# Performance work log

Measured on AMD Instinct MI355X. Metric: run time of the kernel, lower is better.

The kernel has to match this reference:

```python
import jax, jax.numpy as jnp
import numpy as np

N_BINS = 256
HOP = 80


def _gru(xs, Wih, Whh, bih, bhh, reverse=False):
    """Single-layer unidirectional GRU, PyTorch gate layout (r, z, n).
    xs: (T, B, I); Wih: (3H, I); Whh: (3H, H). Returns (T, B, H)."""
    H = Whh.shape[1]
    gi = jnp.einsum('tbi,gi->tbg', xs, Wih) + bih  # precompute input projections

    def step(h, gi_t):
        gh = h @ Whh.T + bhh
        ir, iz, inn = jnp.split(gi_t, 3, axis=-1)
        hr, hz, hn = jnp.split(gh, 3, axis=-1)
        r = jax.nn.sigmoid(ir + hr)
        z = jax.nn.sigmoid(iz + hz)
        n = jnp.tanh(inn + r * hn)
        h_new = (1.0 - z) * n + z * h
        return h_new, h_new

    h0 = jnp.zeros((xs.shape[1], H), xs.dtype)
    _, ys = jax.lax.scan(step, h0, gi, reverse=reverse)
    return ys


def _quantize(w):
    # continuous [-1, 1] -> bin index in [0, N_BINS-1]
    return jnp.clip(jnp.floor((w + 1.0) * (N_BINS / 2)), 0, N_BINS - 1).astype(jnp.int32)


def _forward(x, y, p):
    # --- encode: 2-layer bidirectional GRU over mel frames ---
    c = x
    for l in ('m0', 'm1'):
        f = _gru(c, p[l + 'f_Wih'], p[l + 'f_Whh'], p[l + 'f_bih'], p[l + 'f_bhh'])
        bwd = _gru(c, p[l + 'b_Wih'], p[l + 'b_Whh'], p[l + 'b_bih'], p[l + 'b_bhh'], reverse=True)
        c = jnp.concatenate([f, bwd], axis=-1)  # (t_m, b, 2*dim_enc)
    # nearest-neighbor upsample in time (matches F.interpolate default 'nearest')
    c = jnp.repeat(c, HOP, axis=0)  # (t_w, b, 2*dim_enc)

    # --- teacher forcing: shift waveform right, vectorize via embedding ---
    b = x.shape[1]
    w = jnp.concatenate([jnp.zeros((1, b), y.dtype), y[:-1]], axis=0)
    e = p['E'][_quantize(w)]  # (t_w, b, dim_vec)

    # --- wav GRU + projection + GELU ---
    o = _gru(jnp.concatenate([e, c], axis=-1), p['w_Wih'], p['w_Whh'], p['w_bih'], p['w_bhh'])
    o = jax.nn.gelu(o @ p['Wp'].T + p['bp'], approximate=False)  # (t_w, b, dim_proj)

    # --- categorical neg log prob over quantized targets ---
    logits = o @ p['Wd'].T + p['bd']  # (t_w, b, N_BINS)
    logp = jax.nn.log_softmax(logits, axis=-1)
    tgt = _quantize(y)
    nll = -jnp.mean(jnp.take_along_axis(logp, tgt[..., None], axis=-1))
    return nll


def setup_inputs() -> dict:
    key = jax.random.key(0)
    ks = iter(jax.random.split(key, 64))

    def rn(shape, s=0.08):
        return jax.random.normal(next(ks), shape, jnp.float32) * s

    t_m, b, dm = 32, 4, 80
    de, dv, dd, dp = 128, 256, 896, 512
    d = {}
    d['x'] = jax.random.normal(next(ks), (t_m, b, dm), jnp.float32)
    d['y'] = jax.random.uniform(next(ks), (t_m * HOP, b), jnp.float32, minval=-1.0, maxval=1.0)
    for name, i in [('m0f', dm), ('m0b', dm), ('m1f', 2 * de), ('m1b', 2 * de)]:
        d[name + '_Wih'] = rn((3 * de, i))
        d[name + '_Whh'] = rn((3 * de, de))
        d[name + '_bih'] = rn((3 * de,))
        d[name + '_bhh'] = rn((3 * de,))
    d['w_Wih'] = rn((3 * dd, 2 * de + dv))
    d['w_Whh'] = rn((3 * dd, dd))
    d['w_bih'] = rn((3 * dd,))
    d['w_bhh'] = rn((3 * dd,))
    d['Wp'] = rn((dp, dd))
    d['bp'] = rn((dp,))
    d['E'] = rn((N_BINS, dv))
    d['Wd'] = rn((N_BINS, dp))
    d['bd'] = rn((N_BINS,))
    return d


def reference(x, y, m0f_Wih, m0f_Whh, m0f_bih, m0f_bhh, m0b_Wih, m0b_Whh, m0b_bih, m0b_bhh,
              m1f_Wih, m1f_Whh, m1f_bih, m1f_bhh, m1b_Wih, m1b_Whh, m1b_bih, m1b_bhh,
              w_Wih, w_Whh, w_bih, w_bhh, Wp, bp, E, Wd, bd):
    p = dict(m0f_Wih=m0f_Wih, m0f_Whh=m0f_Whh, m0f_bih=m0f_bih, m0f_bhh=m0f_bhh,
             m0b_Wih=m0b_Wih, m0b_Whh=m0b_Whh, m0b_bih=m0b_bih, m0b_bhh=m0b_bhh,
             m1f_Wih=m1f_Wih, m1f_Whh=m1f_Whh, m1f_bih=m1f_bih, m1f_bhh=m1f_bhh,
             m1b_Wih=m1b_Wih, m1b_Whh=m1b_Whh, m1b_bih=m1b_bih, m1b_bhh=m1b_bhh,
             w_Wih=w_Wih, w_Whh=w_Whh, w_bih=w_bih, w_bhh=w_bhh,
             Wp=Wp, bp=bp, E=E, Wd=Wd, bd=bd)
    return _forward(x, y, p)
```

## Files before the change

### kernel.cpp

```cpp
#include <hip/hip_runtime.h>
#include <stdint.h>
#include <math.h>

typedef __attribute__((ext_vector_type(8))) short bf16x8;
typedef __attribute__((ext_vector_type(4))) float f32x4;
typedef __attribute__((ext_vector_type(4))) unsigned int u32x4;

#define BATCH 4
#define T_M 32
#define DE 128
#define T_W 2560
#define NWG 56

__device__ __forceinline__ float b2f(unsigned short h) {
  return __uint_as_float(((unsigned int)h) << 16);
}
__device__ __forceinline__ unsigned short f2b(float f) {
  unsigned int u = __float_as_uint(f);
  u = u + 0x7fffu + ((u >> 16) & 1u);
  return (unsigned short)(u >> 16);
}
__device__ __forceinline__ float blo(unsigned int u){ return __uint_as_float(u << 16); }
__device__ __forceinline__ float bhi(unsigned int u){ return __uint_as_float(u & 0xffff0000u); }
__device__ __forceinline__ float sigm(float x){
  return __builtin_amdgcn_rcpf(1.f + __expf(-x));
}
__device__ __forceinline__ float tanh_fast(float x){
  float x2 = fminf(fmaxf(x + x, -30.f), 30.f);
  return 1.f - 2.f * __builtin_amdgcn_rcpf(__expf(x2) + 1.f);
}
__device__ __forceinline__ float gelu_exact(float x){ return 0.5f * x * (1.f + erff(x * 0.70710678118654752f)); }

__global__ __launch_bounds__(256) void k_prep(
    const float* __restrict__ wih, const float* __restrict__ wp,
    const float* __restrict__ wd, const float* __restrict__ e,
    const float* __restrict__ whh,
    unsigned short* __restrict__ wih_b, unsigned short* __restrict__ wp_b,
    unsigned short* __restrict__ wd_b, unsigned short* __restrict__ eb,
    unsigned short* __restrict__ whh_p)
{
  int idx = blockIdx.x * 256 + threadIdx.x;
  const int N0 = 2688 * 512, N1 = 512 * 896, N2 = 256 * 512, N3 = 256 * 256;
  if (idx < N0) { wih_b[idx] = f2b(wih[idx]); return; }
  idx -= N0;
  if (idx < N1) { wp_b[idx] = f2b(wp[idx]); return; }
  idx -= N1;
  if (idx < N2) { wd_b[idx] = f2b(wd[idx]); return; }
  idx -= N2;
  if (idx < N3) { eb[idx] = f2b(e[idx]); return; }
  idx -= N3;
  if (idx >= 224 * 28 * 512) return;
  int j    = idx & 7;
  int r16  = (idx >> 3) & 15;
  int quad = (idx >> 7) & 3;
  int kc   = (idx >> 9) % 28;
  int G    = (idx >> 9) / 28;
  unsigned short val = 0;
  if (r16 < 12) {
    int row = (r16 >> 2) * 896 + G * 4 + (r16 & 3);
    int col = kc * 32 + quad * 8 + j;
    val = f2b(whh[(size_t)row * 896 + col]);
  }
  whh_p[idx] = val;
}

__global__ __launch_bounds__(384) void k_gi_enc2(
    const float* __restrict__ in,
    const float* __restrict__ Wih_f, const float* __restrict__ bih_f,
    const float* __restrict__ Wih_b, const float* __restrict__ bih_b,
    float* __restrict__ out_f, float* __restrict__ out_b, int K)
{
  __shared__ float in_s[256];
  int tb = blockIdx.x;
  const float* Wih = blockIdx.y ? Wih_b : Wih_f;
  const float* bih = blockIdx.y ? bih_b : bih_f;
  float* out       = blockIdx.y ? out_b : out_f;
  for (int i = threadIdx.x; i < K; i += 384) in_s[i] = in[tb * K + i];
  __syncthreads();
  int row = threadIdx.x;
  float acc = bih[row];
  const float* wr = Wih + row * K;
  for (int k = 0; k < K; k += 4) {
    float4 w = *(const float4*)(wr + k);
    float4 v = *(const float4*)(in_s + k);
    acc += w.x * v.x + w.y * v.y + w.z * v.z + w.w * v.w;
  }
  out[tb * 384 + row] = acc;
}

__global__ __launch_bounds__(512) void k_scan_enc(
    const float* __restrict__ gi_f, const float* __restrict__ gi_b,
    const float* __restrict__ whh_f, const float* __restrict__ bhh_f,
    const float* __restrict__ whh_b, const float* __restrict__ bhh_b,
    float* __restrict__ c_out, unsigned short* __restrict__ cb)
{
  const int dir = blockIdx.x, tid = threadIdx.x;
  const float* gi  = dir ? gi_b  : gi_f;
  const float* whh = dir ? whh_b : whh_f;
  const float* bhh = dir ? bhh_b : bhh_f;
  __shared__ unsigned short h_s[BATCH][DE + 8];
  __shared__ float gh_s[384][4];
  __shared__ float bhh_s[384];
  for (int i = tid; i < 384; i += 512) bhh_s[i] = bhh[i];
  for (int i = tid; i < BATCH * (DE + 8); i += 512) ((unsigned short*)h_s)[i] = 0;
  __syncthreads();
  for (int s = 0; s < T_M; ++s) {
    int t = dir ? (T_M - 1 - s) : s;
    #pragma unroll
    for (int k3 = 0; k3 < 3; ++k3) {
      int d = tid + 512 * k3;
      int row = d >> 2, b = d & 3;
      const float* wr = whh + row * DE;
      float acc = 0.f;
      for (int j = 0; j < DE; j += 8) {
        float4 w0 = *(const float4*)(wr + j);
        float4 w1 = *(const float4*)(wr + j + 4);
        uint4  hv = *(const uint4*)&h_s[b][j];
        acc += w0.x * blo(hv.x) + w0.y * bhi(hv.x) + w0.z * blo(hv.y) + w0.w * bhi(hv.y);
        acc += w1.x * blo(hv.z) + w1.y * bhi(hv.z) + w1.z * blo(hv.w) + w1.w * bhi(hv.w);
      }
      gh_s[row][b] = acc + bhh_s[row];
    }
    __syncthreads();
    {
      int u = tid >> 2, b = tid & 3;
      const float* git = gi + (t * BATCH + b) * 384;
      float r = sigm(git[u] + gh_s[u][b]);
      float z = sigm(git[DE + u] + gh_s[DE + u][b]);
      float n = tanh_fast(git[2 * DE + u] + r * gh_s[2 * DE + u][b]);
      float hold = b2f(h_s[b][u]);
      float hnew = (1.f - z) * n + z * hold;
      int oi = (t * BATCH + b) * 256 + dir * DE + u;
      c_out[oi] = hnew;
      if (cb) cb[oi] = f2b(hnew);
      h_s[b][u] = f2b(hnew);
    }
    __syncthreads();
  }
}

__global__ __launch_bounds__(256) void k_mgemm(
    const unsigned short* __restrict__ A, const unsigned short* __restrict__ B,
    const float* __restrict__ bias, void* __restrict__ C,
    int M, int N, int K, int act, int c_bf16, int swz, int afuse,
    const unsigned short* __restrict__ Eb, const unsigned short* __restrict__ c1b,
    const float* __restrict__ yw)
{
  __shared__ unsigned short As[128][40];
  __shared__ unsigned short Bs[128][40];
  __shared__ unsigned short Cs[128][136];
  const int tid = threadIdx.x;
  const int m0 = blockIdx.x * 128, n0 = blockIdx.y * 128;
  const int lane = tid & 63, wave = tid >> 6;
  const int wy = wave >> 1, wx = wave & 1;
  const int row16 = lane & 15, quad = lane >> 4;
  const int sr = tid >> 1, sc = (tid & 1) * 16;
  const unsigned short* arow0 = nullptr;
  const unsigned short* arow1 = nullptr;
  if (afuse) {
    int row = m0 + sr, tt = row >> 2, b = row & 3;
    float w = (tt == 0) ? 0.f : yw[(tt - 1) * 4 + b];
    int q = (int)floorf((w + 1.f) * 128.f);
    q = q < 0 ? 0 : (q > 255 ? 255 : q);
    arow0 = Eb + q * 256;
    arow1 = c1b + ((tt / 80) * 4 + b) * 256;
  }
  f32x4 acc[4][4] = {};
  for (int kt = 0; kt < K; kt += 32) {
    uint4 av, av2;
    if (afuse) {
      int kk = kt + sc;
      const unsigned short* src = (kk < 256) ? (arow0 + kk) : (arow1 + kk - 256);
      av  = *(const uint4*)src;
      av2 = *(const uint4*)(src + 8);
    } else {
      av  = *(const uint4*)(A + (size_t)(m0 + sr) * K + kt + sc);
      av2 = *(const uint4*)(A + (size_t)(m0 + sr) * K + kt + sc + 8);
    }
    uint4 bv  = *(const uint4*)(B + (size_t)(n0 + sr) * K + kt + sc);
    uint4 bv2 = *(const uint4*)(B + (size_t)(n0 + sr) * K + kt + sc + 8);
    __syncthreads();
    *(uint4*)&As[sr][sc] = av; *(uint4*)&As[sr][sc + 8] = av2;
    *(uint4*)&Bs[sr][sc] = bv; *(uint4*)&Bs[sr][sc + 8] = bv2;
    __syncthreads();
    bf16x8 af[4], bf[4];
    #pragma unroll
    for (int i = 0; i < 4; ++i) af[i] = *(const bf16x8*)&As[wy * 64 + i * 16 + row16][quad * 8];
    #pragma unroll
    for (int j = 0; j < 4; ++j) bf[j] = *(const bf16x8*)&Bs[wx * 64 + j * 16 + row16][quad * 8];
    #pragma unroll
    for (int i = 0; i < 4; ++i)
      #pragma unroll
      for (int j = 0; j < 4; ++j)
        acc[i][j] = __builtin_amdgcn_mfma_f32_16x16x32_bf16(af[i], bf[j], acc[i][j], 0, 0, 0);
  }

  if (swz || c_bf16) {
    #pragma unroll
    for (int i = 0; i < 4; ++i) {
      #pragma unroll
      for (int j = 0; j < 4; ++j) {
        int col = n0 + wx * 64 + j * 16 + row16;
        float bs = bias[col];
        #pragma unroll
        for (int r = 0; r < 4; ++r) {
          float v = acc[i][j][r] + bs;
          if (act) v = gelu_exact(v);
          Cs[wy * 64 + i * 16 + quad * 4 + r][wx * 64 + j * 16 + row16] = f2b(v);
        }
      }
    }
    __syncthreads();
    if (swz) {
      int g = n0 / 896, G0 = (n0 - g * 896) >> 2;
      unsigned short* gout = (unsigned short*)C;
      #pragma unroll
      for (int k = 0; k < 4; ++k) {
        int bid = tid + 256 * k;
        int tt = bid >> 5, Gl = bid & 31;
        uint2 q0 = *(const uint2*)&Cs[tt * 4 + 0][Gl * 4];
        uint2 q1 = *(const uint2*)&Cs[tt * 4 + 1][Gl * 4];
        uint2 q2 = *(const uint2*)&Cs[tt * 4 + 2][Gl * 4];
        uint2 q3 = *(const uint2*)&Cs[tt * 4 + 3][Gl * 4];
        size_t di = ((size_t)(((m0 >> 2) + tt) * 3 + g) * 224 + (G0 + Gl)) * 16;
        *(uint4*)&gout[di]     = make_uint4(q0.x, q0.y, q1.x, q1.y);
        *(uint4*)&gout[di + 8] = make_uint4(q2.x, q2.y, q3.x, q3.y);
      }
    } else {
      unsigned short* co = (unsigned short*)C;
      #pragma unroll
      for (int k = 0; k < 4; ++k) {
        int idx = tid + 256 * k;
        int row = idx >> 3, c16 = (idx & 7) * 16;
        uint4 a = *(const uint4*)&Cs[row][c16];
        uint4 b = *(const uint4*)&Cs[row][c16 + 8];
        *(uint4*)&co[(size_t)(m0 + row) * N + n0 + c16]     = a;
        *(uint4*)&co[(size_t)(m0 + row) * N + n0 + c16 + 8] = b;
      }
    }
  } else {
    #pragma unroll
    for (int i = 0; i < 4; ++i) {
      #pragma unroll
      for (int j = 0; j < 4; ++j) {
        int col = n0 + wx * 64 + j * 16 + row16;
        float bs = bias[col];
        #pragma unroll
        for (int r = 0; r < 4; ++r) {
          int row = m0 + wy * 64 + i * 16 + quad * 4 + r;
          float v = acc[i][j][r] + bs;
          if (act) v = gelu_exact(v);
          ((float*)C)[(size_t)row * N + col] = v;
        }
      }
    }
  }
}

__global__ __launch_bounds__(256, 1) void k_wav_rnn(
    const unsigned short* __restrict__ whh_p,
    const float* __restrict__ bhh,
    const unsigned short* __restrict__ gp_,
    unsigned int* __restrict__ hslots,
    unsigned int* __restrict__ O32)
{
  const int wg = blockIdx.x, tid = threadIdx.x;
  const int lane = tid & 63, wave = tid >> 6;
  const int G = wg * 4 + wave;

  __shared__ unsigned short h_lds[2][4][912];
  __shared__ float phh[4][3][4][4];

  const int r16 = lane & 15, quad = lane >> 4, bb = lane & 3;
  const int fu = (lane >> 2) & 3, fb = lane & 3;

  bf16x8 wf[28];
  {
    const bf16x8* W8 = (const bf16x8*)whh_p + (size_t)G * 28 * 64;
    #pragma unroll
    for (int kc = 0; kc < 28; ++kc)
      wf[kc] = W8[(kc * 4 + quad) * 16 + r16];
  }

  const float br_ = bhh[G * 4 + fu];
  const float bz_ = bhh[896 + G * 4 + fu];
  const float bn_ = bhh[1792 + G * 4 + fu];
  float hprev = 0.f;
  const unsigned short* gl0 = gp_ + (size_t)G * 16 + fb * 4 + fu;
  unsigned short cr = gl0[0], cz = gl0[3584], cn = gl0[7168];

  const int p0 = tid, p1 = tid + 256, p2 = tid + 512;
  const int p3 = (tid < 128) ? tid + 768 : tid;
  const int pb0 = p0 / 224, pG0 = p0 - pb0 * 224;
  const int pb1 = p1 / 224, pG1 = p1 - pb1 * 224;
  const int pb2 = p2 / 224, pG2 = p2 - pb2 * 224;
  const int pb3 = p3 / 224, pG3 = p3 - pb3 * 224;

  const unsigned long long base0 = (unsigned long long)hslots;
  const unsigned long long base1 = base0 + 14336ull;

  for (int t = 0; t < T_W; ++t) {
    const unsigned long long hb = (t & 1) ? base1 : base0;
    unsigned long long a0 = hb + ((unsigned long long)p0 << 4);
    unsigned long long a1 = hb + ((unsigned long long)p1 << 4);
    unsigned long long a2 = hb + ((unsigned long long)p2 << 4);
    unsigned long long a3 = hb + ((unsigned long long)p3 << 4);
    u32x4 s0, s1, s2, s3;
    const unsigned int tg = (unsigned int)t;
    for (;;) {
      asm volatile(
        "global_load_dwordx4 %0, %4, off sc0 sc1\n"
        "global_load_dwordx4 %1, %5, off sc0 sc1\n"
        "global_load_dwordx4 %2, %6, off sc0 sc1\n"
        "global_load_dwordx4 %3, %7, off sc0 sc1\n"
        "s_waitcnt vmcnt(0)"
        : "=&v"(s0), "=&v"(s1), "=&v"(s2), "=&v"(s3)
        : "v"(a0), "v"(a1), "v"(a2), "v"(a3)
        : "memory");
      unsigned int bad = (s0.z ^ tg) | (s1.z ^ tg) | (s2.z ^ tg) | (s3.z ^ tg);
      if (!__any(bad != 0)) break;
    }

    int tn = (t + 1 < T_W) ? (t + 1) : t;
    const unsigned short* gp = gp_ + (size_t)tn * 10752 + G * 16 + fb * 4 + fu;
    unsigned short nr_ = gp[0], nz_ = gp[3584], nn_ = gp[7168];

    *(uint2*)&h_lds[t & 1][pb0][pG0 * 4] = make_uint2(s0.x, s0.y);
    *(uint2*)&h_lds[t & 1][pb1][pG1 * 4] = make_uint2(s1.x, s1.y);
    *(uint2*)&h_lds[t & 1][pb2][pG2 * 4] = make_uint2(s2.x, s2.y);
    *(uint2*)&h_lds[t & 1][pb3][pG3 * 4] = make_uint2(s3.x, s3.y);
    __syncthreads();

    f32x4 ac0 = {}, ac1 = {}, ac2 = {}, ac3 = {};
    #pragma unroll
    for (int kc = 0; kc < 28; kc += 4) {
      bf16x8 h0 = *(const bf16x8*)&h_lds[t & 1][bb][(kc + 0) * 32 + quad * 8];
      bf16x8 h1 = *(const bf16x8*)&h_lds[t & 1][bb][(kc + 1) * 32 + quad * 8];
      bf16x8 h2 = *(const bf16x8*)&h_lds[t & 1][bb][(kc + 2) * 32 + quad * 8];
      bf16x8 h3 = *(const bf16x8*)&h_lds[t & 1][bb][(kc + 3) * 32 + quad * 8];
      ac0 = __builtin_amdgcn_mfma_f32_16x16x32_bf16(wf[kc + 0], h0, ac0, 0, 0, 0);
      ac1 = __builtin_amdgcn_mfma_f32_16x16x32_bf16(wf[kc + 1], h1, ac1, 0, 0, 0);
      ac2 = __builtin_amdgcn_mfma_f32_16x16x32_bf16(wf[kc + 2], h2, ac2, 0, 0, 0);
      ac3 = __builtin_amdgcn_mfma_f32_16x16x32_bf16(wf[kc + 3], h3, ac3, 0, 0, 0);
    }
    f32x4 ac;
    ac[0] = ac0[0] + ac1[0] + ac2[0] + ac3[0];
    ac[1] = ac0[1] + ac1[1] + ac2[1] + ac3[1];
    ac[2] = ac0[2] + ac1[2] + ac2[2] + ac3[2];
    ac[3] = ac0[3] + ac1[3] + ac2[3] + ac3[3];

    if (r16 < 4 && quad < 3)
      *(f32x4*)&phh[wave][quad][r16][0] = ac;
    asm volatile("s_waitcnt lgkmcnt(0)" ::: "memory");

    float pr = phh[wave][0][fb][fu];
    float pz = phh[wave][1][fb][fu];
    float pn = phh[wave][2][fb][fu];
    float r = sigm(b2f(cr) + br_ + pr);
    float z = sigm(b2f(cz) + bz_ + pz);
    float n = tanh_fast(b2f(cn) + bn_ + r * pn);
    float h = (1.f - z) * n + z * hprev;
    hprev = h;
    unsigned int hu = f2b(h);
    cr = nr_; cz = nz_; cn = nn_;

    int b = lane & 3;
    unsigned int u0v = (unsigned int)__shfl((int)hu, 0 + b);
    unsigned int u1v = (unsigned int)__shfl((int)hu, 4 + b);
    unsigned int u2v = (unsigned int)__shfl((int)hu, 8 + b);
    unsigned int u3v = (unsigned int)__shfl((int)hu, 12 + b);
    if (lane < 4) {
      u32x4 pkt;
      pkt.x = (u0v & 0xffffu) | (u1v << 16);
      pkt.y = (u2v & 0xffffu) | (u3v << 16);
      pkt.z = (unsigned int)(t + 1);
      pkt.w = 0u;
      unsigned long long sa = (((t + 1) & 1) ? base1 : base0)
                            + (unsigned long long)((b * 224 + G) << 4);
      asm volatile("global_store_dwordx4 %0, %1, off sc0 sc1"
                   :: "v"(sa), "v"(pkt) : "memory");
      *(uint2*)(O32 + (size_t)(t * 4 + b) * 448 + G * 2) = make_uint2(pkt.x, pkt.y);
    }
  }
}

__global__ __launch_bounds__(256) void k_nll(
    const float* __restrict__ logits, const float* __restrict__ y,
    float* __restrict__ partials)
{
  __shared__ float ps[4];
  int wid = threadIdx.x >> 6, lane = threadIdx.x & 63;
  int row = blockIdx.x * 4 + wid;
  const float* lr = logits + (size_t)row * 256;
  float v0 = lr[lane], v1 = lr[lane + 64], v2 = lr[lane + 128], v3 = lr[lane + 192];
  float mx = fmaxf(fmaxf(v0, v1), fmaxf(v2, v3));
  for (int off = 32; off > 0; off >>= 1) mx = fmaxf(mx, __shfl_xor(mx, off));
  float se = __expf(v0 - mx) + __expf(v1 - mx) + __expf(v2 - mx) + __expf(v3 - mx);
  for (int off = 32; off > 0; off >>= 1) se += __shfl_xor(se, off);
  if (lane == 0) {
    float w = y[row];
    int q = (int)floorf((w + 1.f) * 128.f);
    q = q < 0 ? 0 : (q > 255 ? 255 : q);
    ps[wid] = (logf(se) + mx) - lr[q];
  }
  __syncthreads();
  if (threadIdx.x == 0) partials[blockIdx.x] = ps[0] + ps[1] + ps[2] + ps[3];
}

__global__ __launch_bounds__(256) void k_final(const float* __restrict__ partials,
                                               float* __restrict__ out)
{
  __shared__ float s[4];
  int tid = threadIdx.x;
  float a = 0.f;
  for (int i = tid; i < 2560; i += 256) a += partials[i];
  for (int off = 32; off > 0; off >>= 1) a += __shfl_xor(a, off);
  if ((tid & 63) == 0) s[tid >> 6] = a;
  __syncthreads();
  if (tid == 0) out[0] = (s[0] + s[1] + s[2] + s[3]) * (1.f / 10240.f);
}

extern "C" void kernel_launch(void* const* d_in, const int* in_sizes, int n_in,
                              void* d_out, int out_size, void* d_ws, size_t ws_size,
                              hipStream_t stream)
{
  const float* x       = (const float*)d_in[0];
  const float* y       = (const float*)d_in[1];
  const float* m0f_Wih = (const float*)d_in[2];
  const float* m0f_Whh = (const float*)d_in[3];
  const float* m0f_bih = (const float*)d_in[4];
  const float* m0f_bhh = (const float*)d_in[5];
  const float* m0b_Wih = (const float*)d_in[6];
  const float* m0b_Whh = (const float*)d_in[7];
  const float* m0b_bih = (const float*)d_in[8];
  const float* m0b_bhh = (const float*)d_in[9];
  const float* m1f_Wih = (const float*)d_in[10];
  const float* m1f_Whh = (const float*)d_in[11];
  const float* m1f_bih = (const float*)d_in[12];
  const float* m1f_bhh = (const float*)d_in[13];
  const float* m1b_Wih = (const float*)d_in[14];
  const float* m1b_Whh = (const float*)d_in[15];
  const float* m1b_bih = (const float*)d_in[16];
  const float* m1b_bhh = (const float*)d_in[17];
  const float* w_Wih   = (const float*)d_in[18];
  const float* w_Whh   = (const float*)d_in[19];
  const float* w_bih   = (const float*)d_in[20];
  const float* w_bhh   = (const float*)d_in[21];
  const float* Wp      = (const float*)d_in[22];
  const float* bp      = (const float*)d_in[23];
  const float* E       = (const float*)d_in[24];
  const float* Wd      = (const float*)d_in[25];
  const float* bd      = (const float*)d_in[26];

  char* ws = (char*)d_ws;
  size_t off = 0;
  auto alloc = [&](size_t bytes) -> void* {
    void* p = ws + off;
    off += (bytes + 255) & ~(size_t)255;
    return p;
  };
  unsigned int* hslots = (unsigned int*)alloc(2 * 896 * 16);
  size_t misc_bytes = off;

  float* c0   = (float*)alloc((size_t)32 * 4 * 256 * 4);
  float* c1   = (float*)alloc((size_t)32 * 4 * 256 * 4);
  float* gi0f = (float*)alloc((size_t)32 * 4 * 384 * 4);
  float* gi0b = (float*)alloc((size_t)32 * 4 * 384 * 4);
  float* gi1f = (float*)alloc((size_t)32 * 4 * 384 * 4);
  float* gi1b = (float*)alloc((size_t)32 * 4 * 384 * 4);
  unsigned short* Eb    = (unsigned short*)alloc((size_t)256 * 256 * 2);
  unsigned short* c1b   = (unsigned short*)alloc((size_t)32 * 4 * 256 * 2);
  unsigned short* gpack = (unsigned short*)alloc((size_t)2560 * 3 * 224 * 16 * 2);
  unsigned int*   O32   = (unsigned int*)alloc((size_t)10240 * 448 * 4);
  unsigned short* O2    = (unsigned short*)alloc((size_t)10240 * 512 * 2);
  float*          LG    = (float*)alloc((size_t)10240 * 256 * 4);
  float*          PT    = (float*)alloc((size_t)2560 * 4);
  unsigned short* Wih_b = (unsigned short*)alloc((size_t)2688 * 512 * 2);
  unsigned short* Whh_p = (unsigned short*)alloc((size_t)224 * 28 * 512 * 2);
  unsigned short* Wp_b  = (unsigned short*)alloc((size_t)512 * 896 * 2);
  unsigned short* Wd_b  = (unsigned short*)alloc((size_t)256 * 512 * 2);

  hipMemsetAsync(d_ws, 0, misc_bytes, stream);

  {
    int total = 2688 * 512 + 512 * 896 + 256 * 512 + 256 * 256 + 224 * 28 * 512;
    k_prep<<<(total + 255) / 256, 256, 0, stream>>>(
        w_Wih, Wp, Wd, E, w_Whh, Wih_b, Wp_b, Wd_b, Eb, Whh_p);
  }

  k_gi_enc2<<<dim3(128, 2), 384, 0, stream>>>(x, m0f_Wih, m0f_bih, m0b_Wih, m0b_bih,
                                              gi0f, gi0b, 80);
  k_scan_enc<<<2, 512, 0, stream>>>(gi0f, gi0b, m0f_Whh, m0f_bhh, m0b_Whh, m0b_bhh,
                                    c0, nullptr);
  k_gi_enc2<<<dim3(128, 2), 384, 0, stream>>>(c0, m1f_Wih, m1f_bih, m1b_Wih, m1b_bih,
                                              gi1f, gi1b, 256);
  k_scan_enc<<<2, 512, 0, stream>>>(gi1f, gi1b, m1f_Whh, m1f_bhh, m1b_Whh, m1b_bhh,
                                    c1, c1b);

  k_mgemm<<<dim3(80, 21), 256, 0, stream>>>(nullptr, Wih_b, w_bih, (void*)gpack,
                                            10240, 2688, 512, 0, 1, 1, 1, Eb, c1b, y);

  k_wav_rnn<<<NWG, 256, 0, stream>>>(Whh_p, w_bhh, gpack, hslots, O32);

  k_mgemm<<<dim3(80, 4), 256, 0, stream>>>((const unsigned short*)O32, Wp_b, bp,
                                           (void*)O2, 10240, 512, 896, 1, 1, 0, 0,
                                           nullptr, nullptr, nullptr);
  k_mgemm<<<dim3(80, 2), 256, 0, stream>>>(O2, Wd_b, bd, (void*)LG,
                                           10240, 256, 512, 0, 0, 0, 0,
                                           nullptr, nullptr, nullptr);
  k_nll<<<2560, 256, 0, stream>>>(LG, y, PT);
  k_final<<<1, 256, 0, stream>>>(PT, (float*)d_out);
}
```

Measured before the change: 5.776 ms.

## Overlap wav-GRU input projection GEMM with recurrent scan in one fused launch

The input-projection GEMM and the wave-level GRU scan now run in one persistent kernel. 56 blocks run the recurrence while 168 worker blocks compute gate-input tiles in time order and signal completion through per-tile atomic counters. The scan polls those counters before prefetching each 32-step chunk, so projection work overlaps the latency-bound recurrence instead of preceding it. The encoder scan also caches its recurrent weights in LDS as bf16 rather than rereading fp32 weights from global memory each step. The risks are spin-wait overhead, co-residency assumptions for the blocks, and slightly lower encoder weight precision.

```diff
diff --git a/kernel.cpp b/kernel.cpp
--- a/kernel.cpp
+++ b/kernel.cpp
@@ -10,7 +10,8 @@
 #define T_M 32
 #define DE 128
 #define T_W 2560
-#define NWG 56
+#define NRNN 56
+#define NWRK 168
 
 __device__ __forceinline__ float b2f(unsigned short h) {
   return __uint_as_float(((unsigned int)h) << 16);
@@ -98,10 +99,15 @@
   const float* gi  = dir ? gi_b  : gi_f;
   const float* whh = dir ? whh_b : whh_f;
   const float* bhh = dir ? bhh_b : bhh_f;
+  __shared__ unsigned short wl[384][136];
   __shared__ unsigned short h_s[BATCH][DE + 8];
   __shared__ float gh_s[384][4];
   __shared__ float bhh_s[384];
-  for (int i = tid; i < 384; i += 512) bhh_s[i] = bhh[i];
+  for (int i = tid; i < 384 * 128; i += 512) {
+    int r = i >> 7, c = i & 127;
+    wl[r][c] = f2b(whh[i]);
+  }
+  if (tid < 384) bhh_s[tid] = bhh[tid];
   for (int i = tid; i < BATCH * (DE + 8); i += 512) ((unsigned short*)h_s)[i] = 0;
   __syncthreads();
   for (int s = 0; s < T_M; ++s) {
@@ -110,14 +116,14 @@
     for (int k3 = 0; k3 < 3; ++k3) {
       int d = tid + 512 * k3;
       int row = d >> 2, b = d & 3;
-      const float* wr = whh + row * DE;
       float acc = 0.f;
       for (int j = 0; j < DE; j += 8) {
-        float4 w0 = *(const float4*)(wr + j);
-        float4 w1 = *(const float4*)(wr + j + 4);
-        uint4  hv = *(const uint4*)&h_s[b][j];
-        acc += w0.x * blo(hv.x) + w0.y * bhi(hv.x) + w0.z * blo(hv.y) + w0.w * bhi(hv.y);
-        acc += w1.x * blo(hv.z) + w1.y * bhi(hv.z) + w1.z * blo(hv.w) + w1.w * bhi(hv.w);
+        uint4 wv = *(const uint4*)&wl[row][j];
+        uint4 hv = *(const uint4*)&h_s[b][j];
+        acc += blo(wv.x) * blo(hv.x) + bhi(wv.x) * bhi(hv.x)
+             + blo(wv.y) * blo(hv.y) + bhi(wv.y) * bhi(hv.y)
+             + blo(wv.z) * blo(hv.z) + bhi(wv.z) * bhi(hv.z)
+             + blo(wv.w) * blo(hv.w) + bhi(wv.w) * bhi(hv.w);
       }
       gh_s[row][b] = acc + bhh_s[row];
     }
@@ -142,9 +148,7 @@
 __global__ __launch_bounds__(256) void k_mgemm(
     const unsigned short* __restrict__ A, const unsigned short* __restrict__ B,
     const float* __restrict__ bias, void* __restrict__ C,
-    int M, int N, int K, int act, int c_bf16, int swz, int afuse,
-    const unsigned short* __restrict__ Eb, const unsigned short* __restrict__ c1b,
-    const float* __restrict__ yw)
+    int M, int N, int K, int act, int c_bf16)
 {
   __shared__ unsigned short As[128][40];
   __shared__ unsigned short Bs[128][40];
@@ -155,28 +159,10 @@
   const int wy = wave >> 1, wx = wave & 1;
   const int row16 = lane & 15, quad = lane >> 4;
   const int sr = tid >> 1, sc = (tid & 1) * 16;
-  const unsigned short* arow0 = nullptr;
-  const unsigned short* arow1 = nullptr;
-  if (afuse) {
-    int row = m0 + sr, tt = row >> 2, b = row & 3;
-    float w = (tt == 0) ? 0.f : yw[(tt - 1) * 4 + b];
-    int q = (int)floorf((w + 1.f) * 128.f);
-    q = q < 0 ? 0 : (q > 255 ? 255 : q);
-    arow0 = Eb + q * 256;
-    arow1 = c1b + ((tt / 80) * 4 + b) * 256;
-  }
   f32x4 acc[4][4] = {};
   for (int kt = 0; kt < K; kt += 32) {
-    uint4 av, av2;
-    if (afuse) {
-      int kk = kt + sc;
-      const unsigned short* src = (kk < 256) ? (arow0 + kk) : (arow1 + kk - 256);
-      av  = *(const uint4*)src;
-      av2 = *(const uint4*)(src + 8);
-    } else {
-      av  = *(const uint4*)(A + (size_t)(m0 + sr) * K + kt + sc);
-      av2 = *(const uint4*)(A + (size_t)(m0 + sr) * K + kt + sc + 8);
-    }
+    uint4 av  = *(const uint4*)(A + (size_t)(m0 + sr) * K + kt + sc);
+    uint4 av2 = *(const uint4*)(A + (size_t)(m0 + sr) * K + kt + sc + 8);
     uint4 bv  = *(const uint4*)(B + (size_t)(n0 + sr) * K + kt + sc);
     uint4 bv2 = *(const uint4*)(B + (size_t)(n0 + sr) * K + kt + sc + 8);
     __syncthreads();
@@ -194,10 +180,9 @@
       for (int j = 0; j < 4; ++j)
         acc[i][j] = __builtin_amdgcn_mfma_f32_16x16x32_bf16(af[i], bf[j], acc[i][j], 0, 0, 0);
   }
-
-  if (swz || c_bf16) {
-    #pragma unroll
-    for (int i = 0; i < 4; ++i) {
+  if (c_bf16) {
+    #pragma unroll
+    for (int i = 0; i < 4; ++i)
       #pragma unroll
       for (int j = 0; j < 4; ++j) {
         int col = n0 + wx * 64 + j * 16 + row16;
@@ -209,38 +194,20 @@
           Cs[wy * 64 + i * 16 + quad * 4 + r][wx * 64 + j * 16 + row16] = f2b(v);
         }
       }
-    }
     __syncthreads();
-    if (swz) {
-      int g = n0 / 896, G0 = (n0 - g * 896) >> 2;
-      unsigned short* gout = (unsigned short*)C;
-      #pragma unroll
-      for (int k = 0; k < 4; ++k) {
-        int bid = tid + 256 * k;
-        int tt = bid >> 5, Gl = bid & 31;
-        uint2 q0 = *(const uint2*)&Cs[tt * 4 + 0][Gl * 4];
-        uint2 q1 = *(const uint2*)&Cs[tt * 4 + 1][Gl * 4];
-        uint2 q2 = *(const uint2*)&Cs[tt * 4 + 2][Gl * 4];
-        uint2 q3 = *(const uint2*)&Cs[tt * 4 + 3][Gl * 4];
-        size_t di = ((size_t)(((m0 >> 2) + tt) * 3 + g) * 224 + (G0 + Gl)) * 16;
-        *(uint4*)&gout[di]     = make_uint4(q0.x, q0.y, q1.x, q1.y);
-        *(uint4*)&gout[di + 8] = make_uint4(q2.x, q2.y, q3.x, q3.y);
-      }
-    } else {
-      unsigned short* co = (unsigned short*)C;
-      #pragma unroll
-      for (int k = 0; k < 4; ++k) {
-        int idx = tid + 256 * k;
-        int row = idx >> 3, c16 = (idx & 7) * 16;
-        uint4 a = *(const uint4*)&Cs[row][c16];
-        uint4 b = *(const uint4*)&Cs[row][c16 + 8];
-        *(uint4*)&co[(size_t)(m0 + row) * N + n0 + c16]     = a;
-        *(uint4*)&co[(size_t)(m0 + row) * N + n0 + c16 + 8] = b;
-      }
+    unsigned short* co = (unsigned short*)C;
+    #pragma unroll
+    for (int k = 0; k < 4; ++k) {
+      int idx = tid + 256 * k;
+      int row = idx >> 3, c16 = (idx & 7) * 16;
+      uint4 a = *(const uint4*)&Cs[row][c16];
+      uint4 b = *(const uint4*)&Cs[row][c16 + 8];
+      *(uint4*)&co[(size_t)(m0 + row) * N + n0 + c16]     = a;
+      *(uint4*)&co[(size_t)(m0 + row) * N + n0 + c16 + 8] = b;
     }
   } else {
     #pragma unroll
-    for (int i = 0; i < 4; ++i) {
+    for (int i = 0; i < 4; ++i)
       #pragma unroll
       for (int j = 0; j < 4; ++j) {
         int col = n0 + wx * 64 + j * 16 + row16;
@@ -253,24 +220,110 @@
           ((float*)C)[(size_t)row * N + col] = v;
         }
       }
-    }
-  }
-}
-
-__global__ __launch_bounds__(256, 1) void k_wav_rnn(
+  }
+}
+
+__global__ __launch_bounds__(256, 1) void k_rnn_fused(
     const unsigned short* __restrict__ whh_p,
     const float* __restrict__ bhh,
     const unsigned short* __restrict__ gp_,
     unsigned int* __restrict__ hslots,
-    unsigned int* __restrict__ O32)
-{
-  const int wg = blockIdx.x, tid = threadIdx.x;
-  const int lane = tid & 63, wave = tid >> 6;
-  const int G = wg * 4 + wave;
-
+    unsigned int* __restrict__ O32,
+    const unsigned short* __restrict__ Bw,
+    const float* __restrict__ bias,
+    unsigned short* __restrict__ gout,
+    const unsigned short* __restrict__ Eb, const unsigned short* __restrict__ c1b,
+    const float* __restrict__ yw,
+    int* __restrict__ gdone)
+{
+  __shared__ unsigned short As[128][40];
+  __shared__ unsigned short Bs[128][40];
+  __shared__ unsigned short Cs[128][136];
   __shared__ unsigned short h_lds[2][4][912];
   __shared__ float phh[4][3][4][4];
-
+  __shared__ float pad_[2900];
+  (void)pad_;
+
+  const int tid = threadIdx.x;
+  const int lane = tid & 63, wave = tid >> 6;
+
+  if (blockIdx.x >= NRNN) {
+    const int wy = wave >> 1, wx = wave & 1;
+    const int row16 = lane & 15, quad = lane >> 4;
+    const int sr = tid >> 1, sc = (tid & 1) * 16;
+    const int K = 512;
+    for (int idx = (int)blockIdx.x - NRNN; idx < 1680; idx += NWRK) {
+      int mt = idx / 21, nt = idx - mt * 21;
+      int m0 = mt * 128, n0 = nt * 128;
+      int row = m0 + sr, tt = row >> 2, b = row & 3;
+      float w = (tt == 0) ? 0.f : yw[(tt - 1) * 4 + b];
+      int q = (int)floorf((w + 1.f) * 128.f);
+      q = q < 0 ? 0 : (q > 255 ? 255 : q);
+      const unsigned short* arow0 = Eb + q * 256;
+      const unsigned short* arow1 = c1b + ((tt / 80) * 4 + b) * 256;
+      f32x4 acc[4][4] = {};
+      for (int kt = 0; kt < K; kt += 32) {
+        int kk = kt + sc;
+        const unsigned short* src = (kk < 256) ? (arow0 + kk) : (arow1 + kk - 256);
+        uint4 av  = *(const uint4*)src;
+        uint4 av2 = *(const uint4*)(src + 8);
+        uint4 bv  = *(const uint4*)(Bw + (size_t)(n0 + sr) * K + kt + sc);
+        uint4 bv2 = *(const uint4*)(Bw + (size_t)(n0 + sr) * K + kt + sc + 8);
+        __syncthreads();
+        *(uint4*)&As[sr][sc] = av; *(uint4*)&As[sr][sc + 8] = av2;
+        *(uint4*)&Bs[sr][sc] = bv; *(uint4*)&Bs[sr][sc + 8] = bv2;
+        __syncthreads();
+        bf16x8 af[4], bf[4];
+        #pragma unroll
+        for (int i = 0; i < 4; ++i) af[i] = *(const bf16x8*)&As[wy * 64 + i * 16 + row16][quad * 8];
+        #pragma unroll
+        for (int j = 0; j < 4; ++j) bf[j] = *(const bf16x8*)&Bs[wx * 64 + j * 16 + row16][quad * 8];
+        #pragma unroll
+        for (int i = 0; i < 4; ++i)
+          #pragma unroll
+          for (int j = 0; j < 4; ++j)
+            acc[i][j] = __builtin_amdgcn_mfma_f32_16x16x32_bf16(af[i], bf[j], acc[i][j], 0, 0, 0);
+      }
+      #pragma unroll
+      for (int i = 0; i < 4; ++i)
+        #pragma unroll
+        for (int j = 0; j < 4; ++j) {
+          int col = n0 + wx * 64 + j * 16 + row16;
+          float bs = bias[col];
+          #pragma unroll
+          for (int r = 0; r < 4; ++r)
+            Cs[wy * 64 + i * 16 + quad * 4 + r][wx * 64 + j * 16 + row16] = f2b(acc[i][j][r] + bs);
+        }
+      __syncthreads();
+      int g = n0 / 896, G0 = (n0 - g * 896) >> 2;
+      #pragma unroll
+      for (int k = 0; k < 4; ++k) {
+        int bid2 = tid + 256 * k;
+        int ttl = bid2 >> 5, Gl = bid2 & 31;
+        uint2 q0 = *(const uint2*)&Cs[ttl * 4 + 0][Gl * 4];
+        uint2 q1 = *(const uint2*)&Cs[ttl * 4 + 1][Gl * 4];
+        uint2 q2 = *(const uint2*)&Cs[ttl * 4 + 2][Gl * 4];
+        uint2 q3 = *(const uint2*)&Cs[ttl * 4 + 3][Gl * 4];
+        u32x4 pA, pB;
+        pA.x = q0.x; pA.y = q0.y; pA.z = q1.x; pA.w = q1.y;
+        pB.x = q2.x; pB.y = q2.y; pB.z = q3.x; pB.w = q3.y;
+        size_t di = ((size_t)(((m0 >> 2) + ttl) * 3 + g) * 224 + (G0 + Gl)) * 16;
+        unsigned long long ad = (unsigned long long)(gout + di);
+        asm volatile("global_store_dwordx4 %0, %1, off sc0 sc1\n"
+                     "global_store_dwordx4 %0, %2, off offset:16 sc0 sc1"
+                     :: "v"(ad), "v"(pA), "v"(pB) : "memory");
+      }
+      asm volatile("s_waitcnt vmcnt(0)" ::: "memory");
+      __syncthreads();
+      if (tid == 0)
+        __hip_atomic_fetch_add(gdone + mt, 1, __ATOMIC_RELEASE, __HIP_MEMORY_SCOPE_AGENT);
+      __syncthreads();
+    }
+    return;
+  }
+
+  const int wg = blockIdx.x;
+  const int G = wg * 4 + wave;
   const int r16 = lane & 15, quad = lane >> 4, bb = lane & 3;
   const int fu = (lane >> 2) & 3, fb = lane & 3;
 
@@ -281,13 +334,28 @@
     for (int kc = 0; kc < 28; ++kc)
       wf[kc] = W8[(kc * 4 + quad) * 16 + r16];
   }
-
   const float br_ = bhh[G * 4 + fu];
   const float bz_ = bhh[896 + G * 4 + fu];
   const float bn_ = bhh[1792 + G * 4 + fu];
   float hprev = 0.f;
-  const unsigned short* gl0 = gp_ + (size_t)G * 16 + fb * 4 + fu;
-  unsigned short cr = gl0[0], cz = gl0[3584], cn = gl0[7168];
+
+  {
+    int v; unsigned long long ga = (unsigned long long)gdone;
+    do {
+      asm volatile("global_load_dword %0, %1, off sc0 sc1\ns_waitcnt vmcnt(0)"
+                   : "=&v"(v) : "v"(ga) : "memory");
+    } while (v < 21);
+  }
+  unsigned int cr, cz, cn;
+  {
+    unsigned long long ga = (unsigned long long)(gp_ + (size_t)G * 16 + fb * 4 + fu);
+    asm volatile("global_load_ushort %0, %3, off sc0 sc1\n"
+                 "global_load_ushort %1, %4, off sc0 sc1\n"
+                 "global_load_ushort %2, %5, off sc0 sc1\n"
+                 "s_waitcnt vmcnt(0)"
+                 : "=&v"(cr), "=&v"(cz), "=&v"(cn)
+                 : "v"(ga), "v"(ga + 7168), "v"(ga + 14336) : "memory");
+  }
 
   const int p0 = tid, p1 = tid + 256, p2 = tid + 512;
   const int p3 = (tid < 128) ? tid + 768 : tid;
@@ -321,15 +389,32 @@
       if (!__any(bad != 0)) break;
     }
 
-    int tn = (t + 1 < T_W) ? (t + 1) : t;
-    const unsigned short* gp = gp_ + (size_t)tn * 10752 + G * 16 + fb * 4 + fu;
-    unsigned short nr_ = gp[0], nz_ = gp[3584], nn_ = gp[7168];
+    unsigned int nr = cr, nz = cz, nn = cn;
+    const int hasPf = (t + 1 < T_W);
+    if (hasPf) {
+      if (((t + 1) & 31) == 0) {
+        int mt2 = (t + 1) >> 5; int v;
+        unsigned long long ga = (unsigned long long)(gdone + mt2);
+        do {
+          asm volatile("global_load_dword %0, %1, off sc0 sc1\ns_waitcnt vmcnt(0)"
+                       : "=&v"(v) : "v"(ga) : "memory");
+        } while (v < 21);
+      }
+      unsigned long long ga = (unsigned long long)(gp_ + (size_t)(t + 1) * 10752 + G * 16 + fb * 4 + fu);
+      asm volatile("global_load_ushort %0, %3, off sc0 sc1\n"
+                   "global_load_ushort %1, %4, off sc0 sc1\n"
+                   "global_load_ushort %2, %5, off sc0 sc1"
+                   : "=&v"(nr), "=&v"(nz), "=&v"(nn)
+                   : "v"(ga), "v"(ga + 7168), "v"(ga + 14336) : "memory");
+    }
 
     *(uint2*)&h_lds[t & 1][pb0][pG0 * 4] = make_uint2(s0.x, s0.y);
     *(uint2*)&h_lds[t & 1][pb1][pG1 * 4] = make_uint2(s1.x, s1.y);
     *(uint2*)&h_lds[t & 1][pb2][pG2 * 4] = make_uint2(s2.x, s2.y);
     *(uint2*)&h_lds[t & 1][pb3][pG3 * 4] = make_uint2(s3.x, s3.y);
     __syncthreads();
+    if (hasPf)
+      asm volatile("s_waitcnt vmcnt(0)" : "+v"(nr), "+v"(nz), "+v"(nn) :: "memory");
 
     f32x4 ac0 = {}, ac1 = {}, ac2 = {}, ac3 = {};
     #pragma unroll
@@ -356,13 +441,13 @@
     float pr = phh[wave][0][fb][fu];
     float pz = phh[wave][1][fb][fu];
     float pn = phh[wave][2][fb][fu];
-    float r = sigm(b2f(cr) + br_ + pr);
-    float z = sigm(b2f(cz) + bz_ + pz);
-    float n = tanh_fast(b2f(cn) + bn_ + r * pn);
+    float r = sigm(b2f((unsigned short)cr) + br_ + pr);
+    float z = sigm(b2f((unsigned short)cz) + bz_ + pz);
+    float n = tanh_fast(b2f((unsigned short)cn) + bn_ + r * pn);
     float h = (1.f - z) * n + z * hprev;
     hprev = h;
     unsigned int hu = f2b(h);
-    cr = nr_; cz = nz_; cn = nn_;
+    cr = nr; cz = nz; cn = nn;
 
     int b = lane & 3;
     unsigned int u0v = (unsigned int)__shfl((int)hu, 0 + b);
@@ -459,6 +544,7 @@
     off += (bytes + 255) & ~(size_t)255;
     return p;
   };
+  int*          gdone  = (int*)alloc(80 * sizeof(int));
   unsigned int* hslots = (unsigned int*)alloc(2 * 896 * 16);
   size_t misc_bytes = off;
 
@@ -497,17 +583,14 @@
   k_scan_enc<<<2, 512, 0, stream>>>(gi1f, gi1b, m1f_Whh, m1f_bhh, m1b_Whh, m1b_bhh,
                                     c1, c1b);
 
-  k_mgemm<<<dim3(80, 21), 256, 0, stream>>>(nullptr, Wih_b, w_bih, (void*)gpack,
-                                            10240, 2688, 512, 0, 1, 1, 1, Eb, c1b, y);
-
-  k_wav_rnn<<<NWG, 256, 0, stream>>>(Whh_p, w_bhh, gpack, hslots, O32);
+  k_rnn_fused<<<NRNN + NWRK, 256, 0, stream>>>(
+      Whh_p, w_bhh, gpack, hslots, O32,
+      Wih_b, w_bih, gpack, Eb, c1b, y, gdone);
 
   k_mgemm<<<dim3(80, 4), 256, 0, stream>>>((const unsigned short*)O32, Wp_b, bp,
-                                           (void*)O2, 10240, 512, 896, 1, 1, 0, 0,
-                                           nullptr, nullptr, nullptr);
+                                           (void*)O2, 10240, 512, 896, 1, 1);
   k_mgemm<<<dim3(80, 2), 256, 0, stream>>>(O2, Wd_b, bd, (void*)LG,
-                                           10240, 256, 512, 0, 0, 0, 0,
-                                           nullptr, nullptr, nullptr);
+                                           10240, 256, 512, 0, 0);
   k_nll<<<2560, 256, 0, stream>>>(LG, y, PT);
   k_final<<<1, 256, 0, stream>>>(PT, (float*)d_out);
 }
```

Measured after the change: 7.970 ms. 38.0% more time.
